# Kernel tuning notes

Hardware: AMD Instinct MI355X
Metric: run time of the kernel (lower is better)

Reference implementation:

```python
import jax, jax.numpy as jnp
import numpy as np

N, D_IN, D_H = 8192, 512, 512


def setup_inputs() -> dict:
    key = jax.random.key(0)
    kH, kWq, kbq, kWk, kbk = jax.random.split(key, 5)
    s_in = 1.0 / np.sqrt(D_IN)
    return {
        "H": jax.random.normal(kH, (N, D_IN), dtype=jnp.float32),
        "Wq": jax.random.normal(kWq, (D_IN, D_H), dtype=jnp.float32) * s_in,
        "bq": jax.random.normal(kbq, (D_H,), dtype=jnp.float32) * 0.01,
        "Wk": jax.random.normal(kWk, (D_IN, D_H), dtype=jnp.float32) * s_in,
        "bk": jax.random.normal(kbk, (D_H,), dtype=jnp.float32) * 0.01,
    }


def reference(H, Wq, bq, Wk, bk):
    # H: [N, T]; Q, K: [N, d_h]
    Q = H @ Wq + bq
    K = H @ Wk + bk
    # A: [N, N] raw scores
    A = Q @ K.T
    n = A.shape[0]
    # torch.where(eye, 0, A): zero out the diagonal BEFORE scale/softmax
    A = A.at[jnp.arange(n), jnp.arange(n)].set(0.0)
    A = A / jnp.sqrt(jnp.asarray(K.shape[-1], A.dtype))
    A = jax.nn.softmax(A, axis=-1)
    # aggregate values (= H itself) and add residual
    return A @ H + H
```

## Files before the change

kernel.cpp:

```cpp
#include <hip/hip_runtime.h>
#include <cstdint>
#include <cstddef>

#define GLOBAL_AS __attribute__((address_space(1)))
#define LDS_AS __attribute__((address_space(3)))

typedef __attribute__((ext_vector_type(8))) short short8;
typedef __attribute__((ext_vector_type(4))) float floatx4;
typedef __attribute__((ext_vector_type(2))) long long2v;
typedef __attribute__((ext_vector_type(4))) int int4v;
typedef __attribute__((ext_vector_type(8))) int int8v;

#if defined(__has_builtin)
#if __has_builtin(__builtin_amdgcn_cvt_pk_fp8_f32)
#define HAVE_HW_FP8 1
#endif
#endif

static __device__ __forceinline__ unsigned short f2bf(float f) {
  uint32_t u = __builtin_bit_cast(uint32_t, f);
  u += 0x7fffu + ((u >> 16) & 1u);
  return (unsigned short)(u >> 16);
}

static __device__ __forceinline__ unsigned char f2fp8(float f) {
#ifdef HAVE_HW_FP8
  float c = fminf(fmaxf(f, -448.f), 448.f);
  return (unsigned char)(__builtin_amdgcn_cvt_pk_fp8_f32(c, 0.f, 0, false) & 0xff);
#else
  unsigned char s = 0;
  if (f < 0.f) { s = 0x80; f = -f; }
  if (f >= 448.f) return s | 0x7e;
  if (f < 0.015625f) { int r = (int)(f * 512.f + 0.5f); return s | (unsigned char)r; }
  uint32_t u = __builtin_bit_cast(uint32_t, f);
  int e = (int)((u >> 23) & 0xff) - 127;
  uint32_t keep = (u >> 20) & 7, rest = u & 0xfffffu;
  if (rest > 0x80000u || (rest == 0x80000u && (keep & 1))) ++keep;
  if (keep == 8) { keep = 0; ++e; }
  if (e > 8) return s | 0x7e;
  return s | (unsigned char)(((e + 7) << 3) | keep);
#endif
}

static __device__ __forceinline__ uint32_t pack4fp8(const float e[4]) {
#ifdef HAVE_HW_FP8
  const uint32_t p01 = (uint32_t)__builtin_amdgcn_cvt_pk_fp8_f32(e[0], e[1], 0, false);
  const uint32_t p23 = (uint32_t)__builtin_amdgcn_cvt_pk_fp8_f32(e[2], e[3], 0, false);
  return (p01 & 0xffffu) | (p23 << 16);
#else
  return (uint32_t)f2fp8(e[0]) | ((uint32_t)f2fp8(e[1]) << 8) |
         ((uint32_t)f2fp8(e[2]) << 16) | ((uint32_t)f2fp8(e[3]) << 24);
#endif
}


static __device__ __forceinline__ void wait_vm0() {
  __builtin_amdgcn_s_waitcnt(0x0f70);
}

static __device__ __forceinline__ int8v load_frag32(const unsigned char* base, int row, int quad) {
  const int h = row & 7;
  const int c0 = (2 * quad) ^ h;
  const int c1 = (2 * quad + 1) ^ h;
  const int4v lo = *(const int4v*)(base + row * 128 + c0 * 16);
  const int4v hi = *(const int4v*)(base + row * 128 + c1 * 16);
  int8v r;
  r[0] = lo[0]; r[1] = lo[1]; r[2] = lo[2]; r[3] = lo[3];
  r[4] = hi[0]; r[5] = hi[1]; r[6] = hi[2]; r[7] = hi[3];
  return r;
}

static __device__ __forceinline__ floatx4 mx_mfma(int8v a, int8v b, floatx4 c) {
  return __builtin_amdgcn_mfma_scale_f32_16x16x128_f8f6f4(a, b, c, 0, 0, 0, 0x7f, 0, 0x7f);
}

__global__ __launch_bounds__(256) void transpose_h_kernel(
    const float* __restrict__ in, unsigned char* __restrict__ outT8,
    unsigned short* __restrict__ outN, int R, int C) {
  __shared__ float t[64][65];
  const int bc = blockIdx.x * 64;
  const int br = blockIdx.y * 64;
  const int tc = threadIdx.x & 63;
  const int tr = threadIdx.x >> 6;
  for (int r = tr; r < 64; r += 4) {
    const float v = in[(size_t)(br + r) * C + bc + tc];
    t[r][tc] = v;
    outN[(size_t)(br + r) * C + bc + tc] = f2bf(v);
  }
  __syncthreads();
  const int tperm = 4 * (tc & 15) + (tc >> 4);
  for (int r = tr; r < 64; r += 4)
    outT8[(size_t)(bc + r) * R + br + tperm] = f2fp8(t[tc][r]);
}

__global__ __launch_bounds__(256) void transpose_w_kernel(
    const float* __restrict__ in, unsigned short* __restrict__ outT, int R, int C) {
  __shared__ float t[64][65];
  const int bc = blockIdx.x * 64;
  const int br = blockIdx.y * 64;
  const int tc = threadIdx.x & 63;
  const int tr = threadIdx.x >> 6;
  for (int r = tr; r < 64; r += 4)
    t[r][tc] = in[(size_t)(br + r) * C + bc + tc];
  __syncthreads();
  for (int r = tr; r < 64; r += 4)
    outT[(size_t)(bc + r) * R + br + tc] = f2bf(t[tc][r]);
}

__global__ __launch_bounds__(256) void pack_bias_kernel(
    const float* __restrict__ bq, const float* __restrict__ bk,
    float* __restrict__ bqk) {
  int i = blockIdx.x * 256 + threadIdx.x;
  bqk[i] = (i < 512) ? bq[i] : bk[i - 512];
}

__global__ __launch_bounds__(256, 4) void gemm_proj(
    const unsigned short* __restrict__ A,
    const unsigned short* __restrict__ Bt,
    int Ncols, int K,
    const float* __restrict__ bias,
    unsigned char* __restrict__ C8)
{
  __shared__ unsigned short As[2][128 * 32];
  __shared__ unsigned short Bs[2][128 * 32];

  const int tid  = threadIdx.x;
  const int lane = tid & 63;
  const int wave = tid >> 6;
  const int wr   = (wave >> 1) * 64;
  const int wc   = (wave & 1) * 64;
  const int quad = lane >> 4;
  const int l15  = lane & 15;
  const int bm   = blockIdx.y * 128;
  const int bn   = blockIdx.x * 128;

  const int c0 = tid, c1 = tid + 256;
  const int r0a = c0 >> 2, k0a = (((c0 & 3) ^ ((c0 >> 3) & 3)) << 3);
  const int r1a = c1 >> 2, k1a = (((c1 & 3) ^ ((c1 >> 3) & 3)) << 3);

  auto stage = [&](int kt, int b) {
    __builtin_amdgcn_global_load_lds(
        (const GLOBAL_AS void*)(A + (size_t)(bm + r0a) * K + kt + k0a),
        (LDS_AS void*)(&As[b][c0 * 8]), 16, 0, 0);
    __builtin_amdgcn_global_load_lds(
        (const GLOBAL_AS void*)(A + (size_t)(bm + r1a) * K + kt + k1a),
        (LDS_AS void*)(&As[b][c1 * 8]), 16, 0, 0);
    __builtin_amdgcn_global_load_lds(
        (const GLOBAL_AS void*)(Bt + (size_t)(bn + r0a) * K + kt + k0a),
        (LDS_AS void*)(&Bs[b][c0 * 8]), 16, 0, 0);
    __builtin_amdgcn_global_load_lds(
        (const GLOBAL_AS void*)(Bt + (size_t)(bn + r1a) * K + kt + k1a),
        (LDS_AS void*)(&Bs[b][c1 * 8]), 16, 0, 0);
  };

  floatx4 acc[4][4];
#pragma unroll
  for (int i = 0; i < 4; ++i)
#pragma unroll
    for (int j = 0; j < 4; ++j)
      acc[i][j] = (floatx4){0.f, 0.f, 0.f, 0.f};

  stage(0, 0);
  const int swq = quad ^ ((l15 >> 1) & 3);
  const int nIter = K >> 5;
  for (int it = 0; it < nIter; ++it) {
    const int b = it & 1;
    wait_vm0();
    __syncthreads();
    if (it + 1 < nIter) stage((it + 1) << 5, b ^ 1);

    short8 af[4], bfr[4];
#pragma unroll
    for (int i = 0; i < 4; ++i)
      af[i] = *(const short8*)(&As[b][(wr + i * 16 + l15) * 32 + swq * 8]);
#pragma unroll
    for (int j = 0; j < 4; ++j)
      bfr[j] = *(const short8*)(&Bs[b][(wc + j * 16 + l15) * 32 + swq * 8]);
#pragma unroll
    for (int i = 0; i < 4; ++i)
#pragma unroll
      for (int j = 0; j < 4; ++j)
        acc[i][j] = __builtin_amdgcn_mfma_f32_16x16x32_bf16(af[i], bfr[j], acc[i][j], 0, 0, 0);
  }

#pragma unroll
  for (int i = 0; i < 4; ++i) {
    const int rl = bm + wr + i * 16 + quad * 4;
#pragma unroll
    for (int r = 0; r < 4; ++r) {
      const int row = rl + r;
      float e[4];
#pragma unroll
      for (int j = 0; j < 4; ++j)
        e[j] = acc[i][j][r] + bias[bn + wc + j * 16 + l15];
      const uint32_t d = pack4fp8(e);
      *(uint32_t*)(C8 + (size_t)row * Ncols + bn + wc + 4 * l15) = d;
    }
  }
}

__global__ __launch_bounds__(256, 4) void gemm_qk8(
    const unsigned char* __restrict__ A,
    const unsigned char* __restrict__ Bt,
    int Ncols, int K, int lda, int ldb,
    float* __restrict__ lsum,
    int row0,
    unsigned char* __restrict__ P8)
{
  __shared__ unsigned char As[2][128 * 64];
  __shared__ unsigned char Bs[2][128 * 64];

  const int tid  = threadIdx.x;
  const int lane = tid & 63;
  const int wave = tid >> 6;
  const int wr   = (wave >> 1) * 64;
  const int wc   = (wave & 1) * 64;
  const int quad = lane >> 4;
  const int l15  = lane & 15;
  const int bm   = blockIdx.y * 128;
  const int bn   = blockIdx.x * 128;

  const int c0 = tid, c1 = tid + 256;
  const int r0a = c0 >> 2, k0a = (((c0 & 3) ^ ((c0 >> 3) & 3)) << 4);
  const int r1a = c1 >> 2, k1a = (((c1 & 3) ^ ((c1 >> 3) & 3)) << 4);

  auto stage = [&](int kt, int b) {
    __builtin_amdgcn_global_load_lds(
        (const GLOBAL_AS void*)(A + (size_t)(bm + r0a) * lda + kt + k0a),
        (LDS_AS void*)(&As[b][c0 * 16]), 16, 0, 0);
    __builtin_amdgcn_global_load_lds(
        (const GLOBAL_AS void*)(A + (size_t)(bm + r1a) * lda + kt + k1a),
        (LDS_AS void*)(&As[b][c1 * 16]), 16, 0, 0);
    __builtin_amdgcn_global_load_lds(
        (const GLOBAL_AS void*)(Bt + (size_t)(bn + r0a) * ldb + kt + k0a),
        (LDS_AS void*)(&Bs[b][c0 * 16]), 16, 0, 0);
    __builtin_amdgcn_global_load_lds(
        (const GLOBAL_AS void*)(Bt + (size_t)(bn + r1a) * ldb + kt + k1a),
        (LDS_AS void*)(&Bs[b][c1 * 16]), 16, 0, 0);
  };

  floatx4 acc[4][4];
#pragma unroll
  for (int i = 0; i < 4; ++i)
#pragma unroll
    for (int j = 0; j < 4; ++j)
      acc[i][j] = (floatx4){0.f, 0.f, 0.f, 0.f};

  stage(0, 0);
  const int swq = quad ^ ((l15 >> 1) & 3);
  const int nIter = K >> 6;
  for (int it = 0; it < nIter; ++it) {
    const int b = it & 1;
    wait_vm0();
    __syncthreads();
    if (it + 1 < nIter) stage((it + 1) << 6, b ^ 1);

    long2v af[4], bfr[4];
#pragma unroll
    for (int i = 0; i < 4; ++i)
      af[i] = *(const long2v*)(&As[b][(wr + i * 16 + l15) * 64 + swq * 16]);
#pragma unroll
    for (int j = 0; j < 4; ++j)
      bfr[j] = *(const long2v*)(&Bs[b][(wc + j * 16 + l15) * 64 + swq * 16]);
#pragma unroll
    for (int i = 0; i < 4; ++i)
#pragma unroll
      for (int j = 0; j < 4; ++j) {
        acc[i][j] = __builtin_amdgcn_mfma_f32_16x16x32_fp8_fp8(af[i].x, bfr[j].x, acc[i][j], 0, 0, 0);
        acc[i][j] = __builtin_amdgcn_mfma_f32_16x16x32_fp8_fp8(af[i].y, bfr[j].y, acc[i][j], 0, 0, 0);
      }
  }

  const float scale = 0.044194173824159216f;
#pragma unroll
  for (int i = 0; i < 4; ++i) {
    const int rl = bm + wr + i * 16 + quad * 4;
#pragma unroll
    for (int r = 0; r < 4; ++r) {
      const int row = rl + r;
      float e[4];
#pragma unroll
      for (int j = 0; j < 4; ++j) {
        const int col = bn + wc + j * 16 + l15;
        const float lg = ((row0 + row) == col) ? 0.f : acc[i][j][r] * scale;
        e[j] = fminf(__expf(lg), 448.f);
      }
      float rsum = (e[0] + e[1]) + (e[2] + e[3]);
      const uint32_t d = pack4fp8(e);
      *(uint32_t*)(P8 + (size_t)row * Ncols + bn + wc + 4 * l15) = d;
      rsum += __shfl_xor(rsum, 1);
      rsum += __shfl_xor(rsum, 2);
      rsum += __shfl_xor(rsum, 4);
      rsum += __shfl_xor(rsum, 8);
      if (l15 == 0) atomicAdd(&lsum[row0 + row], rsum);
    }
  }
}

template <bool DIRECT>
__global__ __launch_bounds__(256, 3) void gemm_pv8(
    const unsigned char* __restrict__ P,
    const unsigned char* __restrict__ Bt,
    int Kchunk,
    const float* __restrict__ lvec,
    const float* __restrict__ Hres,
    int row0,
    float* __restrict__ outp,
    size_t partStride)
{
  __shared__ unsigned char As[2][64 * 128];
  __shared__ unsigned char Bs[2][128 * 128];

  const int tid  = threadIdx.x;
  const int lane = tid & 63;
  const int wave = tid >> 6;
  const int wr   = (wave >> 1) * 32;
  const int wc   = (wave & 1) * 64;
  const int quad = lane >> 4;
  const int l15  = lane & 15;
  const int bm   = blockIdx.y * 64;
  const int bn   = blockIdx.x * 128;
  const int k0   = blockIdx.z * Kchunk;

  float* part = outp + (DIRECT ? 0 : (size_t)blockIdx.z * partStride);

  const int a0 = tid, a1 = tid + 256;
  const int ar0 = a0 >> 3, ac0 = ((a0 & 7) ^ (ar0 & 7)) << 4;
  const int ar1 = a1 >> 3, ac1 = ((a1 & 7) ^ (ar1 & 7)) << 4;
  const int b0 = tid, b1 = tid + 256, b2 = tid + 512, b3 = tid + 768;
  const int br0 = b0 >> 3, bc0 = ((b0 & 7) ^ (br0 & 7)) << 4;
  const int br1 = b1 >> 3, bc1 = ((b1 & 7) ^ (br1 & 7)) << 4;
  const int br2 = b2 >> 3, bc2 = ((b2 & 7) ^ (br2 & 7)) << 4;
  const int br3 = b3 >> 3, bc3 = ((b3 & 7) ^ (br3 & 7)) << 4;

  auto stage = [&](int kt, int b) {
    __builtin_amdgcn_global_load_lds(
        (const GLOBAL_AS void*)(P + (size_t)(bm + ar0) * 8192 + kt + ac0),
        (LDS_AS void*)(&As[b][a0 * 16]), 16, 0, 0);
    __builtin_amdgcn_global_load_lds(
        (const GLOBAL_AS void*)(P + (size_t)(bm + ar1) * 8192 + kt + ac1),
        (LDS_AS void*)(&As[b][a1 * 16]), 16, 0, 0);
    __builtin_amdgcn_global_load_lds(
        (const GLOBAL_AS void*)(Bt + (size_t)(bn + br0) * 8192 + kt + bc0),
        (LDS_AS void*)(&Bs[b][b0 * 16]), 16, 0, 0);
    __builtin_amdgcn_global_load_lds(
        (const GLOBAL_AS void*)(Bt + (size_t)(bn + br1) * 8192 + kt + bc1),
        (LDS_AS void*)(&Bs[b][b1 * 16]), 16, 0, 0);
    __builtin_amdgcn_global_load_lds(
        (const GLOBAL_AS void*)(Bt + (size_t)(bn + br2) * 8192 + kt + bc2),
        (LDS_AS void*)(&Bs[b][b2 * 16]), 16, 0, 0);
    __builtin_amdgcn_global_load_lds(
        (const GLOBAL_AS void*)(Bt + (size_t)(bn + br3) * 8192 + kt + bc3),
        (LDS_AS void*)(&Bs[b][b3 * 16]), 16, 0, 0);
  };

  floatx4 acc[2][4];
#pragma unroll
  for (int i = 0; i < 2; ++i)
#pragma unroll
    for (int j = 0; j < 4; ++j)
      acc[i][j] = (floatx4){0.f, 0.f, 0.f, 0.f};

  stage(k0, 0);
  const int nIter = Kchunk >> 7;
  for (int it = 0; it < nIter; ++it) {
    const int b = it & 1;
    wait_vm0();
    __syncthreads();
    if (it + 1 < nIter) stage(k0 + ((it + 1) << 7), b ^ 1);

    const int8v af0 = load_frag32(As[b], wr + l15, quad);
    const int8v af1 = load_frag32(As[b], wr + 16 + l15, quad);
#pragma unroll
    for (int j = 0; j < 4; ++j) {
      const int8v bf = load_frag32(Bs[b], wc + j * 16 + l15, quad);
      acc[0][j] = mx_mfma(af0, bf, acc[0][j]);
      acc[1][j] = mx_mfma(af1, bf, acc[1][j]);
    }
  }

#pragma unroll
  for (int i = 0; i < 2; ++i) {
    const int rl = bm + wr + i * 16 + quad * 4;
#pragma unroll
    for (int j = 0; j < 4; ++j) {
      const int col = bn + wc + j * 16 + l15;
#pragma unroll
      for (int r = 0; r < 4; ++r) {
        const int row = rl + r;
        const float v = acc[i][j][r];
        if (DIRECT) {
          const int grow = row0 + row;
          part[(size_t)grow * 512 + col] =
              v / lvec[grow] + Hres[(size_t)grow * 512 + col];
        } else {
          part[(size_t)row * 512 + col] = v;
        }
      }
    }
  }
}

__global__ __launch_bounds__(256) void combine_kernel(
    const float* __restrict__ parts, size_t partStride, int S,
    const float* __restrict__ lvec, const float* __restrict__ Hres,
    float* __restrict__ out, int n4) {
  int i = blockIdx.x * 256 + threadIdx.x;
  if (i >= n4) return;
  float4 a = ((const float4*)parts)[i];
  for (int s = 1; s < S; ++s) {
    const float4 b = ((const float4*)(parts + (size_t)s * partStride))[i];
    a.x += b.x; a.y += b.y; a.z += b.z; a.w += b.w;
  }
  const int row = i >> 7;
  const float inv = 1.f / lvec[row];
  const float4 h = ((const float4*)Hres)[i];
  float4 o;
  o.x = a.x * inv + h.x;
  o.y = a.y * inv + h.y;
  o.z = a.z * inv + h.z;
  o.w = a.w * inv + h.w;
  ((float4*)out)[i] = o;
}

extern "C" void kernel_launch(void* const* d_in, const int* in_sizes, int n_in,
                              void* d_out, int out_size, void* d_ws, size_t ws_size,
                              hipStream_t stream) {
  const float* H  = (const float*)d_in[0];
  const float* Wq = (const float*)d_in[1];
  const float* bq = (const float*)d_in[2];
  const float* Wk = (const float*)d_in[3];
  const float* bk = (const float*)d_in[4];
  float* out = (float*)d_out;

  const int N = 8192, D = 512;

  char* ws = (char*)d_ws;
  size_t off = 0;
  auto alloc = [&](size_t bytes) { char* p = ws + off; off += bytes; return p; };
  unsigned short* Hb   = (unsigned short*)alloc((size_t)N * D * 2);
  unsigned char*  HbT8 = (unsigned char*)alloc((size_t)D * N);
  unsigned char*  QK8  = (unsigned char*)alloc((size_t)N * 2 * D);
  unsigned short* BqkT = (unsigned short*)alloc((size_t)2 * D * D * 2);
  float* bqk = (float*)alloc((size_t)2 * D * 4);
  float* l   = (float*)alloc((size_t)N * 4);
  const size_t base = off;
  unsigned char* P8 = (unsigned char*)(ws + base);

  const size_t pBytes = (size_t)N * N;
  const size_t partBytes = (size_t)N * D * 4;
  const size_t partStride = (size_t)N * D;
  const size_t avail = (ws_size > base) ? (ws_size - base) : 0;

  int S = 0;
  if (avail >= pBytes) {
    const size_t extra = avail - pBytes;
    S = (extra >= 2 * partBytes) ? 2 : 1;
  }
  float* parts = (float*)(ws + base + pBytes);

  hipMemsetAsync(l, 0, (size_t)N * 4, stream);
  transpose_h_kernel<<<dim3(D / 64, N / 64), 256, 0, stream>>>(H, HbT8, Hb, N, D);
  transpose_w_kernel<<<dim3(D / 64, D / 64), 256, 0, stream>>>(Wq, BqkT, D, D);
  transpose_w_kernel<<<dim3(D / 64, D / 64), 256, 0, stream>>>(Wk, BqkT + (size_t)D * D, D, D);
  pack_bias_kernel<<<dim3(4), 256, 0, stream>>>(bq, bk, bqk);

  gemm_proj<<<dim3(2 * D / 128, N / 128), 256, 0, stream>>>(
      Hb, BqkT, 2 * D, D, bqk, QK8);

  if (S >= 1) {
    gemm_qk8<<<dim3(N / 128, N / 128), 256, 0, stream>>>(
        QK8, QK8 + D, N, D, 2 * D, 2 * D, l, 0, P8);
    if (S == 1) {
      gemm_pv8<true><<<dim3(D / 128, N / 64, 1), 256, 0, stream>>>(
          P8, HbT8, N, l, H, 0, out, 0);
    } else {
      gemm_pv8<false><<<dim3(D / 128, N / 64, S), 256, 0, stream>>>(
          P8, HbT8, N / S, nullptr, nullptr, 0, parts, partStride);
      combine_kernel<<<dim3((N * D / 4 + 255) / 256), 256, 0, stream>>>(
          parts, partStride, S, l, H, out, N * D / 4);
    }
  } else {
    int maxRows = (int)(avail / (size_t)N);
    maxRows &= ~127;
    if (maxRows < 128) maxRows = 128;
    for (int r0 = 0; r0 < N; r0 += maxRows) {
      int rows = N - r0;
      if (rows > maxRows) rows = maxRows;
      gemm_qk8<<<dim3(N / 128, rows / 128), 256, 0, stream>>>(
          QK8 + (size_t)r0 * 2 * D, QK8 + D, N, D, 2 * D, 2 * D, l, r0, P8);
      gemm_pv8<true><<<dim3(D / 128, rows / 64, 1), 256, 0, stream>>>(
          P8, HbT8, N, l, H, r0, out, 0);
    }
  }
}
```

Measured before the change: 257.6 us.

## Triple-buffer QK GEMM pipeline and use scaled 16x16x128 FP8 MFMA

Reworks the main loop of the QK FP8 GEMM to walk K in 128-wide super-steps over a three-slot LDS ring. Two 64-wide K slices are kept in flight, using partial vmcnt waits and scheduling barriers instead of a full drain each step. Each super-step feeds one mfma_scale 16x16x128 instruction per output tile instead of two 16x16x32 FP8 MFMAs, and raises wave priority during the MFMA burst. This costs more LDS per block, so the occupancy hint drops from 4 to 3 blocks per CU.

```diff
diff --git a/kernel.cpp b/kernel.cpp
--- a/kernel.cpp
+++ b/kernel.cpp
@@ -57,6 +57,15 @@
 static __device__ __forceinline__ void wait_vm0() {
   __builtin_amdgcn_s_waitcnt(0x0f70);
 }
+static __device__ __forceinline__ void wait_vm4() {
+  __builtin_amdgcn_s_waitcnt(0x0f74);
+}
+static __device__ __forceinline__ void wait_lgkm0() {
+  __builtin_amdgcn_s_waitcnt(0xC07F);
+}
+static __device__ __forceinline__ void sfence() {
+  __builtin_amdgcn_sched_barrier(0);
+}
 
 static __device__ __forceinline__ int8v load_frag32(const unsigned char* base, int row, int quad) {
   const int h = row & 7;
@@ -64,6 +73,13 @@
   const int c1 = (2 * quad + 1) ^ h;
   const int4v lo = *(const int4v*)(base + row * 128 + c0 * 16);
   const int4v hi = *(const int4v*)(base + row * 128 + c1 * 16);
+  int8v r;
+  r[0] = lo[0]; r[1] = lo[1]; r[2] = lo[2]; r[3] = lo[3];
+  r[4] = hi[0]; r[5] = hi[1]; r[6] = hi[2]; r[7] = hi[3];
+  return r;
+}
+
+static __device__ __forceinline__ int8v cat8(int4v lo, int4v hi) {
   int8v r;
   r[0] = lo[0]; r[1] = lo[1]; r[2] = lo[2]; r[3] = lo[3];
   r[4] = hi[0]; r[5] = hi[1]; r[6] = hi[2]; r[7] = hi[3];
@@ -199,7 +215,7 @@
   }
 }
 
-__global__ __launch_bounds__(256, 4) void gemm_qk8(
+__global__ __launch_bounds__(256, 3) void gemm_qk8(
     const unsigned char* __restrict__ A,
     const unsigned char* __restrict__ Bt,
     int Ncols, int K, int lda, int ldb,
@@ -207,8 +223,8 @@
     int row0,
     unsigned char* __restrict__ P8)
 {
-  __shared__ unsigned char As[2][128 * 64];
-  __shared__ unsigned char Bs[2][128 * 64];
+  __shared__ unsigned char As[3][128 * 64];
+  __shared__ unsigned char Bs[3][128 * 64];
 
   const int tid  = threadIdx.x;
   const int lane = tid & 63;
@@ -247,28 +263,52 @@
       acc[i][j] = (floatx4){0.f, 0.f, 0.f, 0.f};
 
   stage(0, 0);
+  stage(64, 1);
+
   const int swq = quad ^ ((l15 >> 1) & 3);
-  const int nIter = K >> 6;
-  for (int it = 0; it < nIter; ++it) {
-    const int b = it & 1;
-    wait_vm0();
-    __syncthreads();
-    if (it + 1 < nIter) stage((it + 1) << 6, b ^ 1);
-
-    long2v af[4], bfr[4];
+  const int nSuper = K >> 7;
+  int e = 0, o = 1, n = 2;
+  int4v aLo[4], bLo[4];
+
+  for (int s = 0; s < nSuper; ++s) {
+    const bool more = (s + 1 < nSuper);
+    sfence();
+    __builtin_amdgcn_s_barrier();
+    wait_vm4();
+    sfence();
+    if (more) stage((s << 7) + 128, n);
 #pragma unroll
     for (int i = 0; i < 4; ++i)
-      af[i] = *(const long2v*)(&As[b][(wr + i * 16 + l15) * 64 + swq * 16]);
+      aLo[i] = *(const int4v*)(&As[e][(wr + i * 16 + l15) * 64 + swq * 16]);
 #pragma unroll
     for (int j = 0; j < 4; ++j)
-      bfr[j] = *(const long2v*)(&Bs[b][(wc + j * 16 + l15) * 64 + swq * 16]);
+      bLo[j] = *(const int4v*)(&Bs[e][(wc + j * 16 + l15) * 64 + swq * 16]);
+    wait_lgkm0();
+    sfence();
+    __builtin_amdgcn_s_barrier();
+    if (more) { wait_vm4(); } else { wait_vm0(); }
+    sfence();
+    if (more) stage((s << 7) + 192, e);
+    int4v aHi[4], bHi[4];
 #pragma unroll
     for (int i = 0; i < 4; ++i)
-#pragma unroll
-      for (int j = 0; j < 4; ++j) {
-        acc[i][j] = __builtin_amdgcn_mfma_f32_16x16x32_fp8_fp8(af[i].x, bfr[j].x, acc[i][j], 0, 0, 0);
-        acc[i][j] = __builtin_amdgcn_mfma_f32_16x16x32_fp8_fp8(af[i].y, bfr[j].y, acc[i][j], 0, 0, 0);
-      }
+      aHi[i] = *(const int4v*)(&As[o][(wr + i * 16 + l15) * 64 + swq * 16]);
+#pragma unroll
+    for (int j = 0; j < 4; ++j)
+      bHi[j] = *(const int4v*)(&Bs[o][(wc + j * 16 + l15) * 64 + swq * 16]);
+
+    __builtin_amdgcn_s_setprio(1);
+#pragma unroll
+    for (int i = 0; i < 4; ++i) {
+      const int8v a8 = cat8(aLo[i], aHi[i]);
+#pragma unroll
+      for (int j = 0; j < 4; ++j)
+        acc[i][j] = mx_mfma(a8, cat8(bLo[j], bHi[j]), acc[i][j]);
+    }
+    __builtin_amdgcn_s_setprio(0);
+
+    const int oe = e, oo = o;
+    e = n; o = oe; n = oo;
   }
 
   const float scale = 0.044194173824159216f;
@@ -278,15 +318,15 @@
 #pragma unroll
     for (int r = 0; r < 4; ++r) {
       const int row = rl + r;
-      float e[4];
+      float e4[4];
 #pragma unroll
       for (int j = 0; j < 4; ++j) {
         const int col = bn + wc + j * 16 + l15;
         const float lg = ((row0 + row) == col) ? 0.f : acc[i][j][r] * scale;
-        e[j] = fminf(__expf(lg), 448.f);
+        e4[j] = fminf(__expf(lg), 448.f);
       }
-      float rsum = (e[0] + e[1]) + (e[2] + e[3]);
-      const uint32_t d = pack4fp8(e);
+      float rsum = (e4[0] + e4[1]) + (e4[2] + e4[3]);
+      const uint32_t d = pack4fp8(e4);
       *(uint32_t*)(P8 + (size_t)row * Ncols + bn + wc + 4 * l15) = d;
       rsum += __shfl_xor(rsum, 1);
       rsum += __shfl_xor(rsum, 2);
```

After: 265.3 us. +3.0%, slower.

## Switch QK fp8 GEMM to 32x32x64 scaled MFMA tiles

Applied to the files above, without the earlier changes.

Replaces the 16x16x32 fp8 MFMA inner loop of the QK score kernel with the 32x32x64 scaled f8f6f4 MFMA, using 2x2 accumulators of 16 floats per wave. Fragment loading, the epilogue row/column mapping and the fp8 column permutation in the H transpose are changed together so the packed P layout stays consistent for the PV kernel. The aim is fewer MFMA issues and LDS reads per k-step. In exchange, the epilogue writes 2-byte stores instead of 4-byte ones and adds one more shuffle step to the row-sum reduction.

```diff
diff --git a/kernel.cpp b/kernel.cpp
--- a/kernel.cpp
+++ b/kernel.cpp
@@ -7,7 +7,7 @@
 
 typedef __attribute__((ext_vector_type(8))) short short8;
 typedef __attribute__((ext_vector_type(4))) float floatx4;
-typedef __attribute__((ext_vector_type(2))) long long2v;
+typedef __attribute__((ext_vector_type(16))) float floatx16;
 typedef __attribute__((ext_vector_type(4))) int int4v;
 typedef __attribute__((ext_vector_type(8))) int int8v;
 
@@ -53,6 +53,14 @@
 #endif
 }
 
+static __device__ __forceinline__ unsigned short pack2fp8(float a, float b) {
+#ifdef HAVE_HW_FP8
+  return (unsigned short)(__builtin_amdgcn_cvt_pk_fp8_f32(a, b, 0, false) & 0xffffu);
+#else
+  return (unsigned short)((uint32_t)f2fp8(a) | ((uint32_t)f2fp8(b) << 8));
+#endif
+}
+
 
 static __device__ __forceinline__ void wait_vm0() {
   __builtin_amdgcn_s_waitcnt(0x0f70);
@@ -70,8 +78,19 @@
   return r;
 }
 
+static __device__ __forceinline__ int8v cat8(int4v lo, int4v hi) {
+  int8v r;
+  r[0] = lo[0]; r[1] = lo[1]; r[2] = lo[2]; r[3] = lo[3];
+  r[4] = hi[0]; r[5] = hi[1]; r[6] = hi[2]; r[7] = hi[3];
+  return r;
+}
+
 static __device__ __forceinline__ floatx4 mx_mfma(int8v a, int8v b, floatx4 c) {
   return __builtin_amdgcn_mfma_scale_f32_16x16x128_f8f6f4(a, b, c, 0, 0, 0, 0x7f, 0, 0x7f);
+}
+
+static __device__ __forceinline__ floatx16 mx_mfma32(int8v a, int8v b, floatx16 c) {
+  return __builtin_amdgcn_mfma_scale_f32_32x32x64_f8f6f4(a, b, c, 0, 0, 0, 0x7f, 0, 0x7f);
 }
 
 __global__ __launch_bounds__(256) void transpose_h_kernel(
@@ -88,7 +107,7 @@
     outN[(size_t)(br + r) * C + bc + tc] = f2bf(v);
   }
   __syncthreads();
-  const int tperm = 4 * (tc & 15) + (tc >> 4);
+  const int tperm = 2 * (tc & 31) + (tc >> 5);
   for (int r = tr; r < 64; r += 4)
     outT8[(size_t)(bc + r) * R + br + tperm] = f2fp8(t[tc][r]);
 }
@@ -215,8 +234,8 @@
   const int wave = tid >> 6;
   const int wr   = (wave >> 1) * 64;
   const int wc   = (wave & 1) * 64;
-  const int quad = lane >> 4;
-  const int l15  = lane & 15;
+  const int l31  = lane & 31;
+  const int half = lane >> 5;
   const int bm   = blockIdx.y * 128;
   const int bn   = blockIdx.x * 128;
 
@@ -239,15 +258,16 @@
         (LDS_AS void*)(&Bs[b][c1 * 16]), 16, 0, 0);
   };
 
-  floatx4 acc[4][4];
-#pragma unroll
-  for (int i = 0; i < 4; ++i)
-#pragma unroll
-    for (int j = 0; j < 4; ++j)
-      acc[i][j] = (floatx4){0.f, 0.f, 0.f, 0.f};
+  floatx16 acc[2][2];
+#pragma unroll
+  for (int i = 0; i < 2; ++i)
+#pragma unroll
+    for (int j = 0; j < 2; ++j)
+      acc[i][j] = (floatx16)0.f;
 
   stage(0, 0);
-  const int swq = quad ^ ((l15 >> 1) & 3);
+  const int chLo = (((half << 1) ^ ((l31 >> 1) & 3)) << 4);
+  const int chHi = chLo ^ 16;
   const int nIter = K >> 6;
   for (int it = 0; it < nIter; ++it) {
     const int b = it & 1;
@@ -255,44 +275,45 @@
     __syncthreads();
     if (it + 1 < nIter) stage((it + 1) << 6, b ^ 1);
 
-    long2v af[4], bfr[4];
-#pragma unroll
-    for (int i = 0; i < 4; ++i)
-      af[i] = *(const long2v*)(&As[b][(wr + i * 16 + l15) * 64 + swq * 16]);
-#pragma unroll
-    for (int j = 0; j < 4; ++j)
-      bfr[j] = *(const long2v*)(&Bs[b][(wc + j * 16 + l15) * 64 + swq * 16]);
-#pragma unroll
-    for (int i = 0; i < 4; ++i)
-#pragma unroll
-      for (int j = 0; j < 4; ++j) {
-        acc[i][j] = __builtin_amdgcn_mfma_f32_16x16x32_fp8_fp8(af[i].x, bfr[j].x, acc[i][j], 0, 0, 0);
-        acc[i][j] = __builtin_amdgcn_mfma_f32_16x16x32_fp8_fp8(af[i].y, bfr[j].y, acc[i][j], 0, 0, 0);
-      }
+    int8v aF[2], bF[2];
+#pragma unroll
+    for (int i = 0; i < 2; ++i) {
+      const unsigned char* rp = &As[b][(wr + i * 32 + l31) * 64];
+      aF[i] = cat8(*(const int4v*)(rp + chLo), *(const int4v*)(rp + chHi));
+    }
+#pragma unroll
+    for (int j = 0; j < 2; ++j) {
+      const unsigned char* rp = &Bs[b][(wc + j * 32 + l31) * 64];
+      bF[j] = cat8(*(const int4v*)(rp + chLo), *(const int4v*)(rp + chHi));
+    }
+#pragma unroll
+    for (int i = 0; i < 2; ++i)
+#pragma unroll
+      for (int j = 0; j < 2; ++j)
+        acc[i][j] = mx_mfma32(aF[i], bF[j], acc[i][j]);
   }
 
   const float scale = 0.044194173824159216f;
 #pragma unroll
-  for (int i = 0; i < 4; ++i) {
-    const int rl = bm + wr + i * 16 + quad * 4;
-#pragma unroll
-    for (int r = 0; r < 4; ++r) {
-      const int row = rl + r;
-      float e[4];
-#pragma unroll
-      for (int j = 0; j < 4; ++j) {
-        const int col = bn + wc + j * 16 + l15;
-        const float lg = ((row0 + row) == col) ? 0.f : acc[i][j][r] * scale;
-        e[j] = fminf(__expf(lg), 448.f);
-      }
-      float rsum = (e[0] + e[1]) + (e[2] + e[3]);
-      const uint32_t d = pack4fp8(e);
-      *(uint32_t*)(P8 + (size_t)row * Ncols + bn + wc + 4 * l15) = d;
+  for (int i = 0; i < 2; ++i) {
+#pragma unroll
+    for (int r = 0; r < 16; ++r) {
+      const int row = bm + wr + i * 32 + (r & 3) + 8 * (r >> 2) + 4 * half;
+      const int cg0 = bn + wc + l31;
+      const int cg1 = cg0 + 32;
+      const float lg0 = ((row0 + row) == cg0) ? 0.f : acc[i][0][r] * scale;
+      const float lg1 = ((row0 + row) == cg1) ? 0.f : acc[i][1][r] * scale;
+      const float e0 = fminf(__expf(lg0), 448.f);
+      const float e1 = fminf(__expf(lg1), 448.f);
+      *(unsigned short*)(P8 + (size_t)row * Ncols + bn + wc + 2 * l31) =
+          pack2fp8(e0, e1);
+      float rsum = e0 + e1;
       rsum += __shfl_xor(rsum, 1);
       rsum += __shfl_xor(rsum, 2);
       rsum += __shfl_xor(rsum, 4);
       rsum += __shfl_xor(rsum, 8);
-      if (l15 == 0) atomicAdd(&lsum[row0 + row], rsum);
+      rsum += __shfl_xor(rsum, 16);
+      if (l31 == 0) atomicAdd(&lsum[row0 + row], rsum);
     }
   }
 }
```

After: 295.0 us. 1.15x slower.
